# Optimization experiments

Measured on AMD Instinct MI355X. Metric: run time of the kernel, lower is better.

## Reference

```python
import jax, jax.numpy as jnp
import numpy as np

NUM_CLUSTERS = 64
DIM = 512
ALPHA = 100.0
EPS = 1e-12  # torch F.normalize eps


def setup_inputs() -> dict:
    key = jax.random.key(0)
    k1, k2 = jax.random.split(key)
    x1 = jax.random.normal(k1, (30, DIM, 28, 28), dtype=jnp.float32)
    centroids = jax.random.uniform(k2, (NUM_CLUSTERS, DIM), dtype=jnp.float32)
    # _init_params: conv weight = 2*alpha*centroids (1x1 conv), bias = -alpha*||centroid||
    conv_w = 2.0 * ALPHA * centroids
    conv_b = -ALPHA * jnp.linalg.norm(centroids, axis=1)
    return {"x1": x1, "centroids": centroids, "conv_w": conv_w, "conv_b": conv_b}


def _l2norm(v, axis):
    n = jnp.sqrt(jnp.sum(v * v, axis=axis, keepdims=True))
    return v / jnp.maximum(n, EPS)


def reference(x1, centroids, conv_w, conv_b):
    T, C, H, W = x1.shape
    K, D = centroids.shape
    x = x1.reshape(T, C, H * W)            # [T, C, N]
    x = _l2norm(x, axis=1)                 # normalize_input: L2 over channel dim
    # 1x1 conv == matmul over channels: logits [T, K, N]
    logits = jnp.einsum('kc,tcn->tkn', conv_w, x) + conv_b[None, :, None]
    a = jax.nn.softmax(logits, axis=1)     # soft assignment over clusters
    # vlad[t,k,c] = sum_n a[t,k,n]*(x[t,c,n] - centroids[k,c])
    # rewritten as two small matmuls, avoiding the [K,C,N] residual tensor
    vlad = jnp.einsum('tkn,tcn->tkc', a, x) - a.sum(axis=-1)[:, :, None] * centroids[None]
    vlad = _l2norm(vlad, axis=2)           # intra-normalization over feature dim
    v = vlad.reshape(T, K * D)
    v = _l2norm(v, axis=1)                 # global L2 normalization
    return v.sum(axis=0, keepdims=True)    # [1, K*D] accumulated over 30 timesteps
```

## Files before the change

kernel.cpp:

```cpp
#include <hip/hip_runtime.h>
#include <math.h>

#define T_ 30
#define C_ 512
#define N_ 784
#define NA_ 800
#define XPITCH 520
#define EPSV 1e-12f

typedef __attribute__((ext_vector_type(8))) short bf16x8;
typedef __attribute__((ext_vector_type(4))) float f32x4;

__device__ __forceinline__ unsigned short f2bf(float f) {
    union { float f; unsigned int u; } v; v.f = f;
    unsigned int r = (v.u + 0x7FFFu + ((v.u >> 16) & 1u)) >> 16;
    return (unsigned short)r;
}
__device__ __forceinline__ float bf2f(unsigned short h) {
    union { unsigned int u; float f; } v; v.u = ((unsigned int)h) << 16;
    return v.f;
}

__global__ void k_prep(const float* __restrict__ w, unsigned short* __restrict__ wh,
                       unsigned short* __restrict__ wl) {
    int idx = blockIdx.x * 256 + threadIdx.x;
    float v = w[idx];
    unsigned short h = f2bf(v);
    wh[idx] = h;
    wl[idx] = f2bf(v - bf2f(h));
}

__global__ __launch_bounds__(256) void k_assign(
    const float* __restrict__ x, const unsigned short* __restrict__ wh,
    const unsigned short* __restrict__ wl, const float* __restrict__ b,
    unsigned short* __restrict__ aT, float* __restrict__ asum)
{
    __shared__ __align__(16) char smem[2 * 16 * XPITCH * 2];
    unsigned short* xh = (unsigned short*)smem;
    unsigned short* xl = xh + 16 * XPITCH;
    float* red = (float*)smem;
    __shared__ float ssq[4][16];
    __shared__ float invl[16];

    int t = blockIdx.y, n0 = blockIdx.x * 16;
    int tid = threadIdx.x;
    int w = tid >> 6, L = tid & 63, lid = L & 15, quad = L >> 4;

    int nseg = (tid & 3) * 4;
    int crow = tid >> 2;
    float ss0 = 0.f, ss1 = 0.f, ss2 = 0.f, ss3 = 0.f;
    #pragma unroll
    for (int p = 0; p < 8; ++p) {
        int c = p * 64 + crow;
        float4 q = *reinterpret_cast<const float4*>(
            x + ((size_t)t * C_ + c) * N_ + n0 + nseg);
        ss0 = fmaf(q.x, q.x, ss0); ss1 = fmaf(q.y, q.y, ss1);
        ss2 = fmaf(q.z, q.z, ss2); ss3 = fmaf(q.w, q.w, ss3);
        float vv[4] = {q.x, q.y, q.z, q.w};
        #pragma unroll
        for (int j = 0; j < 4; ++j) {
            unsigned short h = f2bf(vv[j]);
            xh[(nseg + j) * XPITCH + c] = h;
            xl[(nseg + j) * XPITCH + c] = f2bf(vv[j] - bf2f(h));
        }
    }
    #pragma unroll
    for (int m = 4; m <= 32; m <<= 1) {
        ss0 += __shfl_xor(ss0, m, 64); ss1 += __shfl_xor(ss1, m, 64);
        ss2 += __shfl_xor(ss2, m, 64); ss3 += __shfl_xor(ss3, m, 64);
    }
    if (L < 4) {
        ssq[w][L * 4 + 0] = ss0; ssq[w][L * 4 + 1] = ss1;
        ssq[w][L * 4 + 2] = ss2; ssq[w][L * 4 + 3] = ss3;
    }
    __syncthreads();
    if (tid < 16) {
        float s = ssq[0][tid] + ssq[1][tid] + ssq[2][tid] + ssq[3][tid];
        invl[tid] = 1.0f / fmaxf(sqrtf(s), EPSV);
    }

    f32x4 acc[4];
    #pragma unroll
    for (int mt = 0; mt < 4; ++mt)
        #pragma unroll
        for (int r = 0; r < 4; ++r) acc[mt][r] = 0.f;

    #pragma unroll
    for (int ks = 0; ks < 4; ++ks) {
        int cs = w * 128 + ks * 32;
        bf16x8 bh = *reinterpret_cast<const bf16x8*>(&xh[lid * XPITCH + cs + quad * 8]);
        bf16x8 bl = *reinterpret_cast<const bf16x8*>(&xl[lid * XPITCH + cs + quad * 8]);
        #pragma unroll
        for (int mt = 0; mt < 4; ++mt) {
            bf16x8 ah = *reinterpret_cast<const bf16x8*>(wh + (size_t)(mt * 16 + lid) * C_ + cs + quad * 8);
            bf16x8 al = *reinterpret_cast<const bf16x8*>(wl + (size_t)(mt * 16 + lid) * C_ + cs + quad * 8);
            acc[mt] = __builtin_amdgcn_mfma_f32_16x16x32_bf16(ah, bh, acc[mt], 0, 0, 0);
            acc[mt] = __builtin_amdgcn_mfma_f32_16x16x32_bf16(al, bh, acc[mt], 0, 0, 0);
            acc[mt] = __builtin_amdgcn_mfma_f32_16x16x32_bf16(ah, bl, acc[mt], 0, 0, 0);
        }
    }
    __syncthreads();
    {
        float* rp = red + w * (16 * 68);
        #pragma unroll
        for (int mt = 0; mt < 4; ++mt)
            *reinterpret_cast<f32x4*>(&rp[lid * 68 + mt * 16 + quad * 4]) = acc[mt];
    }
    __syncthreads();

    float bk = b[L];
    float asl = 0.f;
    unsigned short av[4];
    #pragma unroll
    for (int i = 0; i < 4; ++i) {
        int n = w * 4 + i;
        float v = red[0 * 1088 + n * 68 + L] + red[1 * 1088 + n * 68 + L]
                + red[2 * 1088 + n * 68 + L] + red[3 * 1088 + n * 68 + L];
        float inv = invl[n];
        v = fmaf(v, inv, bk);
        float mx = v;
        #pragma unroll
        for (int m = 1; m <= 32; m <<= 1) mx = fmaxf(mx, __shfl_xor(mx, m, 64));
        float e = __expf(v - mx);
        float se = e;
        #pragma unroll
        for (int m = 1; m <= 32; m <<= 1) se += __shfl_xor(se, m, 64);
        float a = e / se;
        av[i] = f2bf(a * inv);
        asl += a;
    }
    atomicAdd(&asum[t * 64 + L], asl);
    ushort4 st; st.x = av[0]; st.y = av[1]; st.z = av[2]; st.w = av[3];
    *reinterpret_cast<ushort4*>(aT + ((size_t)t * 64 + L) * NA_ + n0 + w * 4) = st;
}

__global__ __launch_bounds__(256) void k_vlad(
    const float* __restrict__ x, const unsigned short* __restrict__ aT,
    const float* __restrict__ asum, const float* __restrict__ cent,
    float* __restrict__ vlad, float* __restrict__ g2)
{
    __shared__ float red[4][16 * 68];
    int t = blockIdx.y, c0 = blockIdx.x * 16;
    int tid = threadIdx.x;
    int w = tid >> 6, L = tid & 63, lid = L & 15, quad = L >> 4;

    f32x4 acc[4];
    #pragma unroll
    for (int mt = 0; mt < 4; ++mt)
        #pragma unroll
        for (int r = 0; r < 4; ++r) acc[mt][r] = 0.f;

    const float* xrow = x + ((size_t)t * C_ + c0 + lid) * N_;
    const unsigned short* ab = aT + (size_t)t * 64 * NA_;

    for (int s = w; s < 25; s += 4) {
        int nb = s * 32 + quad * 8;
        int nbc = nb > 776 ? 776 : nb;
        float4 x0 = *reinterpret_cast<const float4*>(xrow + nbc);
        float4 x1 = *reinterpret_cast<const float4*>(xrow + nbc + 4);
        bf16x8 bb;
        bb[0] = (short)f2bf(x0.x); bb[1] = (short)f2bf(x0.y);
        bb[2] = (short)f2bf(x0.z); bb[3] = (short)f2bf(x0.w);
        bb[4] = (short)f2bf(x1.x); bb[5] = (short)f2bf(x1.y);
        bb[6] = (short)f2bf(x1.z); bb[7] = (short)f2bf(x1.w);
        #pragma unroll
        for (int mt = 0; mt < 4; ++mt) {
            bf16x8 af = *reinterpret_cast<const bf16x8*>(ab + (size_t)(mt * 16 + lid) * NA_ + nb);
            acc[mt] = __builtin_amdgcn_mfma_f32_16x16x32_bf16(af, bb, acc[mt], 0, 0, 0);
        }
    }
    {
        float* rp = &red[w][0];
        #pragma unroll
        for (int mt = 0; mt < 4; ++mt)
            *reinterpret_cast<f32x4*>(&rp[lid * 68 + mt * 16 + quad * 4]) = acc[mt];
    }
    __syncthreads();

    int k = tid >> 2, cs4 = (tid & 3) * 4;
    float as = asum[t * 64 + k];
    float4 cv = *reinterpret_cast<const float4*>(cent + k * C_ + c0 + cs4);
    float4 vout;
    float s2 = 0.f;
    #pragma unroll
    for (int j = 0; j < 4; ++j) {
        int cc = cs4 + j;
        float v = red[0][cc * 68 + k] + red[1][cc * 68 + k]
                + red[2][cc * 68 + k] + red[3][cc * 68 + k];
        v -= as * ((const float*)&cv)[j];
        ((float*)&vout)[j] = v;
        s2 = fmaf(v, v, s2);
    }
    *reinterpret_cast<float4*>(vlad + ((size_t)t * 64 + k) * C_ + c0 + cs4) = vout;
    s2 += __shfl_xor(s2, 1, 64);
    s2 += __shfl_xor(s2, 2, 64);
    if ((tid & 3) == 0) atomicAdd(&g2[t * 64 + k], s2);
}

__global__ __launch_bounds__(256) void k_out(
    const float* __restrict__ vlad, const float* __restrict__ g2,
    float* __restrict__ out)
{
    __shared__ float intr[1920];
    __shared__ float gl[1920];
    __shared__ float sinv[T_];
    int tid = threadIdx.x;
    for (int i = tid; i < 1920; i += 256) {
        float s = g2[i];
        gl[i] = s;
        intr[i] = 1.0f / fmaxf(sqrtf(s), EPSV);
    }
    __syncthreads();
    if (tid < T_) {
        float s = 0.f;
        #pragma unroll 8
        for (int k = 0; k < 64; ++k) {
            float iv = intr[tid * 64 + k];
            s += gl[tid * 64 + k] * iv * iv;
        }
        sinv[tid] = 1.0f / fmaxf(sqrtf(s), EPSV);
    }
    __syncthreads();
    int idx = blockIdx.x * 256 + tid;
    int k = idx >> 9;
    float s = 0.f;
    #pragma unroll 5
    for (int t = 0; t < T_; ++t)
        s += vlad[(size_t)t * 32768 + idx] * intr[t * 64 + k] * sinv[t];
    out[idx] = s;
}

extern "C" void kernel_launch(void* const* d_in, const int* in_sizes, int n_in,
                              void* d_out, int out_size, void* d_ws, size_t ws_size,
                              hipStream_t stream) {
    const float* x    = (const float*)d_in[0];
    const float* cent = (const float*)d_in[1];
    const float* w    = (const float*)d_in[2];
    const float* b    = (const float*)d_in[3];
    float* out = (float*)d_out;

    char* p = (char*)d_ws;
    unsigned short* wh = (unsigned short*)p;  p += 65536;
    unsigned short* wl = (unsigned short*)p;  p += 65536;
    float* asum = (float*)p;                  p += 1920 * 4;
    float* g2   = (float*)p;                  p += 1920 * 4;
    unsigned short* aT = (unsigned short*)p;  p += (size_t)T_ * 64 * NA_ * 2;
    float* vlad = (float*)p;                  p += (size_t)T_ * 64 * C_ * 4;

    k_prep<<<128, 256, 0, stream>>>(w, wh, wl);
    hipMemsetAsync(asum, 0, 2 * 1920 * 4, stream);
    hipMemsetAsync(aT, 0, (size_t)T_ * 64 * NA_ * 2, stream);
    k_assign<<<dim3(49, T_), 256, 0, stream>>>(x, wh, wl, b, aT, asum);
    k_vlad<<<dim3(32, T_), 256, 0, stream>>>(x, aT, asum, cent, vlad, g2);
    k_out<<<128, 256, 0, stream>>>(vlad, g2, out);
}
```

Measured before the change: 150.6 us.

## Prefetch loads in assign and vlad kernels, batch softmax reductions, drop aT memset

```diff
diff --git a/kernel.cpp b/kernel.cpp
--- a/kernel.cpp
+++ b/kernel.cpp
@@ -30,7 +30,7 @@
     wl[idx] = f2bf(v - bf2f(h));
 }
 
-__global__ __launch_bounds__(256) void k_assign(
+__global__ __launch_bounds__(256, 4) void k_assign(
     const float* __restrict__ x, const unsigned short* __restrict__ wh,
     const unsigned short* __restrict__ wl, const float* __restrict__ b,
     unsigned short* __restrict__ aT, float* __restrict__ asum)
@@ -40,23 +40,39 @@
     unsigned short* xl = xh + 16 * XPITCH;
     float* red = (float*)smem;
     __shared__ float ssq[4][16];
-    __shared__ float invl[16];
 
     int t = blockIdx.y, n0 = blockIdx.x * 16;
     int tid = threadIdx.x;
     int w = tid >> 6, L = tid & 63, lid = L & 15, quad = L >> 4;
-
-    int nseg = (tid & 3) * 4;
-    int crow = tid >> 2;
+    int cbase = w * 128;
+    int nseg = (L & 3) * 4;
+    int crow = L >> 2;
+
+    float4 q[8];
+    #pragma unroll
+    for (int p = 0; p < 8; ++p) {
+        int c = cbase + p * 16 + crow;
+        q[p] = *reinterpret_cast<const float4*>(
+            x + ((size_t)t * C_ + c) * N_ + n0 + nseg);
+    }
+    float bk = b[L];
+
+    const unsigned short* wha = wh + (size_t)lid * C_ + cbase + quad * 8;
+    const unsigned short* wla = wl + (size_t)lid * C_ + cbase + quad * 8;
+    bf16x8 cah[4], cal[4];
+    #pragma unroll
+    for (int mt = 0; mt < 4; ++mt) {
+        cah[mt] = *reinterpret_cast<const bf16x8*>(wha + mt * 16 * C_);
+        cal[mt] = *reinterpret_cast<const bf16x8*>(wla + mt * 16 * C_);
+    }
+
     float ss0 = 0.f, ss1 = 0.f, ss2 = 0.f, ss3 = 0.f;
     #pragma unroll
     for (int p = 0; p < 8; ++p) {
-        int c = p * 64 + crow;
-        float4 q = *reinterpret_cast<const float4*>(
-            x + ((size_t)t * C_ + c) * N_ + n0 + nseg);
-        ss0 = fmaf(q.x, q.x, ss0); ss1 = fmaf(q.y, q.y, ss1);
-        ss2 = fmaf(q.z, q.z, ss2); ss3 = fmaf(q.w, q.w, ss3);
-        float vv[4] = {q.x, q.y, q.z, q.w};
+        int c = cbase + p * 16 + crow;
+        float vv[4] = {q[p].x, q[p].y, q[p].z, q[p].w};
+        ss0 = fmaf(vv[0], vv[0], ss0); ss1 = fmaf(vv[1], vv[1], ss1);
+        ss2 = fmaf(vv[2], vv[2], ss2); ss3 = fmaf(vv[3], vv[3], ss3);
         #pragma unroll
         for (int j = 0; j < 4; ++j) {
             unsigned short h = f2bf(vv[j]);
@@ -73,11 +89,6 @@
         ssq[w][L * 4 + 0] = ss0; ssq[w][L * 4 + 1] = ss1;
         ssq[w][L * 4 + 2] = ss2; ssq[w][L * 4 + 3] = ss3;
     }
-    __syncthreads();
-    if (tid < 16) {
-        float s = ssq[0][tid] + ssq[1][tid] + ssq[2][tid] + ssq[3][tid];
-        invl[tid] = 1.0f / fmaxf(sqrtf(s), EPSV);
-    }
 
     f32x4 acc[4];
     #pragma unroll
@@ -87,17 +98,29 @@
 
     #pragma unroll
     for (int ks = 0; ks < 4; ++ks) {
-        int cs = w * 128 + ks * 32;
+        bf16x8 nah[4], nal[4];
+        #pragma unroll
+        for (int mt = 0; mt < 4; ++mt) { nah[mt] = cah[mt]; nal[mt] = cal[mt]; }
+        if (ks < 3) {
+            #pragma unroll
+            for (int mt = 0; mt < 4; ++mt) {
+                nah[mt] = *reinterpret_cast<const bf16x8*>(
+                    wha + mt * 16 * C_ + (ks + 1) * 32);
+                nal[mt] = *reinterpret_cast<const bf16x8*>(
+                    wla + mt * 16 * C_ + (ks + 1) * 32);
+            }
+        }
+        int cs = cbase + ks * 32;
         bf16x8 bh = *reinterpret_cast<const bf16x8*>(&xh[lid * XPITCH + cs + quad * 8]);
         bf16x8 bl = *reinterpret_cast<const bf16x8*>(&xl[lid * XPITCH + cs + quad * 8]);
         #pragma unroll
         for (int mt = 0; mt < 4; ++mt) {
-            bf16x8 ah = *reinterpret_cast<const bf16x8*>(wh + (size_t)(mt * 16 + lid) * C_ + cs + quad * 8);
-            bf16x8 al = *reinterpret_cast<const bf16x8*>(wl + (size_t)(mt * 16 + lid) * C_ + cs + quad * 8);
-            acc[mt] = __builtin_amdgcn_mfma_f32_16x16x32_bf16(ah, bh, acc[mt], 0, 0, 0);
-            acc[mt] = __builtin_amdgcn_mfma_f32_16x16x32_bf16(al, bh, acc[mt], 0, 0, 0);
-            acc[mt] = __builtin_amdgcn_mfma_f32_16x16x32_bf16(ah, bl, acc[mt], 0, 0, 0);
-        }
+            acc[mt] = __builtin_amdgcn_mfma_f32_16x16x32_bf16(cah[mt], bh, acc[mt], 0, 0, 0);
+            acc[mt] = __builtin_amdgcn_mfma_f32_16x16x32_bf16(cal[mt], bh, acc[mt], 0, 0, 0);
+            acc[mt] = __builtin_amdgcn_mfma_f32_16x16x32_bf16(cah[mt], bl, acc[mt], 0, 0, 0);
+        }
+        #pragma unroll
+        for (int mt = 0; mt < 4; ++mt) { cah[mt] = nah[mt]; cal[mt] = nal[mt]; }
     }
     __syncthreads();
     {
@@ -108,30 +131,45 @@
     }
     __syncthreads();
 
-    float bk = b[L];
+    float vv[4], iv[4];
+    #pragma unroll
+    for (int i = 0; i < 4; ++i) {
+        int n = w * 4 + i;
+        float s = ssq[0][n] + ssq[1][n] + ssq[2][n] + ssq[3][n];
+        iv[i] = 1.0f / fmaxf(sqrtf(s), EPSV);
+        float v = red[0 * 1088 + n * 68 + L] + red[1 * 1088 + n * 68 + L]
+                + red[2 * 1088 + n * 68 + L] + red[3 * 1088 + n * 68 + L];
+        vv[i] = fmaf(v, iv[i], bk);
+    }
+    float mx[4] = {vv[0], vv[1], vv[2], vv[3]};
+    #pragma unroll
+    for (int m = 1; m <= 32; m <<= 1) {
+        #pragma unroll
+        for (int i = 0; i < 4; ++i) mx[i] = fmaxf(mx[i], __shfl_xor(mx[i], m, 64));
+    }
+    float e[4], se[4];
+    #pragma unroll
+    for (int i = 0; i < 4; ++i) { e[i] = __expf(vv[i] - mx[i]); se[i] = e[i]; }
+    #pragma unroll
+    for (int m = 1; m <= 32; m <<= 1) {
+        #pragma unroll
+        for (int i = 0; i < 4; ++i) se[i] += __shfl_xor(se[i], m, 64);
+    }
     float asl = 0.f;
     unsigned short av[4];
     #pragma unroll
     for (int i = 0; i < 4; ++i) {
-        int n = w * 4 + i;
-        float v = red[0 * 1088 + n * 68 + L] + red[1 * 1088 + n * 68 + L]
-                + red[2 * 1088 + n * 68 + L] + red[3 * 1088 + n * 68 + L];
-        float inv = invl[n];
-        v = fmaf(v, inv, bk);
-        float mx = v;
-        #pragma unroll
-        for (int m = 1; m <= 32; m <<= 1) mx = fmaxf(mx, __shfl_xor(mx, m, 64));
-        float e = __expf(v - mx);
-        float se = e;
-        #pragma unroll
-        for (int m = 1; m <= 32; m <<= 1) se += __shfl_xor(se, m, 64);
-        float a = e / se;
-        av[i] = f2bf(a * inv);
+        float a = e[i] / se[i];
+        av[i] = f2bf(a * iv[i]);
         asl += a;
     }
     atomicAdd(&asum[t * 64 + L], asl);
     ushort4 st; st.x = av[0]; st.y = av[1]; st.z = av[2]; st.w = av[3];
     *reinterpret_cast<ushort4*>(aT + ((size_t)t * 64 + L) * NA_ + n0 + w * 4) = st;
+    if (blockIdx.x == 48) {
+        ushort4 z; z.x = 0; z.y = 0; z.z = 0; z.w = 0;
+        *reinterpret_cast<ushort4*>(aT + ((size_t)t * 64 + L) * NA_ + 784 + w * 4) = z;
+    }
 }
 
 __global__ __launch_bounds__(256) void k_vlad(
@@ -151,35 +189,54 @@
         for (int r = 0; r < 4; ++r) acc[mt][r] = 0.f;
 
     const float* xrow = x + ((size_t)t * C_ + c0 + lid) * N_;
-    const unsigned short* ab = aT + (size_t)t * 64 * NA_;
-
-    for (int s = w; s < 25; s += 4) {
-        int nb = s * 32 + quad * 8;
-        int nbc = nb > 776 ? 776 : nb;
-        float4 x0 = *reinterpret_cast<const float4*>(xrow + nbc);
-        float4 x1 = *reinterpret_cast<const float4*>(xrow + nbc + 4);
-        bf16x8 bb;
-        bb[0] = (short)f2bf(x0.x); bb[1] = (short)f2bf(x0.y);
-        bb[2] = (short)f2bf(x0.z); bb[3] = (short)f2bf(x0.w);
-        bb[4] = (short)f2bf(x1.x); bb[5] = (short)f2bf(x1.y);
-        bb[6] = (short)f2bf(x1.z); bb[7] = (short)f2bf(x1.w);
-        #pragma unroll
-        for (int mt = 0; mt < 4; ++mt) {
-            bf16x8 af = *reinterpret_cast<const bf16x8*>(ab + (size_t)(mt * 16 + lid) * NA_ + nb);
-            acc[mt] = __builtin_amdgcn_mfma_f32_16x16x32_bf16(af, bb, acc[mt], 0, 0, 0);
-        }
-    }
-    {
-        float* rp = &red[w][0];
-        #pragma unroll
-        for (int mt = 0; mt < 4; ++mt)
-            *reinterpret_cast<f32x4*>(&rp[lid * 68 + mt * 16 + quad * 4]) = acc[mt];
-    }
-    __syncthreads();
+    const unsigned short* a0 = aT + (size_t)t * 64 * NA_ + (size_t)lid * NA_;
 
     int k = tid >> 2, cs4 = (tid & 3) * 4;
     float as = asum[t * 64 + k];
     float4 cv = *reinterpret_cast<const float4*>(cent + k * C_ + c0 + cs4);
+
+    int nb = w * 32 + quad * 8;
+    int nc = nb > 776 ? 776 : nb;
+    float4 x0c = *reinterpret_cast<const float4*>(xrow + nc);
+    float4 x1c = *reinterpret_cast<const float4*>(xrow + nc + 4);
+    bf16x8 f0 = *reinterpret_cast<const bf16x8*>(a0 + nb);
+    bf16x8 f1 = *reinterpret_cast<const bf16x8*>(a0 + 16 * NA_ + nb);
+    bf16x8 f2 = *reinterpret_cast<const bf16x8*>(a0 + 32 * NA_ + nb);
+    bf16x8 f3 = *reinterpret_cast<const bf16x8*>(a0 + 48 * NA_ + nb);
+
+    for (int s = w; s < 25; s += 4) {
+        int sn = s + 4;
+        float4 x0n = x0c, x1n = x1c;
+        bf16x8 g0 = f0, g1 = f1, g2v = f2, g3 = f3;
+        if (sn < 25) {
+            int nb2 = sn * 32 + quad * 8;
+            int nc2 = nb2 > 776 ? 776 : nb2;
+            x0n = *reinterpret_cast<const float4*>(xrow + nc2);
+            x1n = *reinterpret_cast<const float4*>(xrow + nc2 + 4);
+            g0 = *reinterpret_cast<const bf16x8*>(a0 + nb2);
+            g1 = *reinterpret_cast<const bf16x8*>(a0 + 16 * NA_ + nb2);
+            g2v = *reinterpret_cast<const bf16x8*>(a0 + 32 * NA_ + nb2);
+            g3 = *reinterpret_cast<const bf16x8*>(a0 + 48 * NA_ + nb2);
+        }
+        bf16x8 bb;
+        bb[0] = (short)f2bf(x0c.x); bb[1] = (short)f2bf(x0c.y);
+        bb[2] = (short)f2bf(x0c.z); bb[3] = (short)f2bf(x0c.w);
+        bb[4] = (short)f2bf(x1c.x); bb[5] = (short)f2bf(x1c.y);
+        bb[6] = (short)f2bf(x1c.z); bb[7] = (short)f2bf(x1c.w);
+        acc[0] = __builtin_amdgcn_mfma_f32_16x16x32_bf16(f0, bb, acc[0], 0, 0, 0);
+        acc[1] = __builtin_amdgcn_mfma_f32_16x16x32_bf16(f1, bb, acc[1], 0, 0, 0);
+        acc[2] = __builtin_amdgcn_mfma_f32_16x16x32_bf16(f2, bb, acc[2], 0, 0, 0);
+        acc[3] = __builtin_amdgcn_mfma_f32_16x16x32_bf16(f3, bb, acc[3], 0, 0, 0);
+        x0c = x0n; x1c = x1n; f0 = g0; f1 = g1; f2 = g2v; f3 = g3;
+    }
+    {
+        float* rp = &red[w][0];
+        #pragma unroll
+        for (int mt = 0; mt < 4; ++mt)
+            *reinterpret_cast<f32x4*>(&rp[lid * 68 + mt * 16 + quad * 4]) = acc[mt];
+    }
+    __syncthreads();
+
     float4 vout;
     float s2 = 0.f;
     #pragma unroll
@@ -249,7 +306,6 @@
 
     k_prep<<<128, 256, 0, stream>>>(w, wh, wl);
     hipMemsetAsync(asum, 0, 2 * 1920 * 4, stream);
-    hipMemsetAsync(aT, 0, (size_t)T_ * 64 * NA_ * 2, stream);
     k_assign<<<dim3(49, T_), 256, 0, stream>>>(x, wh, wl, b, aT, asum);
     k_vlad<<<dim3(32, T_), 256, 0, stream>>>(x, aT, asum, cent, vlad, g2);
     k_out<<<128, 256, 0, stream>>>(vlad, g2, out);
```

Result: faster. 140.7 us (-6.6%).
